# Optimization experiments

Hardware: AMD Instinct MI355X
Metric: run time of the kernel (lower is better)

Reference implementation:

```python
import jax, jax.numpy as jnp
import numpy as np

ITERATIONS = 3


def squash(s):
    # Faithful to the torch code: norm is taken over axis 2 (the labels axis
    # for s_j of shape (B, 1, L, O)), exactly as torch's squash(dim=2) does.
    mag_sq = jnp.sum(s * s, axis=2, keepdims=True)
    mag = jnp.sqrt(mag_sq)
    return mag_sq / (1.0 + mag_sq) * (s / mag)


def setup_inputs() -> dict:
    key = jax.random.key(0)
    kx, kw = jax.random.split(key)
    B, N, P, L, O = 256, 8, 1152, 10, 16
    x = jax.random.normal(kx, (B, N, P), dtype=jnp.float32)
    # nn.Parameter(torch.randn(1, P, L, O, N))
    W = jax.random.normal(kw, (1, P, L, O, N), dtype=jnp.float32)
    return {"x": x, "W": W}


def reference(x, W):
    # x: (B, N, P), W: (1, P, L, O, N)
    _, P, L, O, N = W.shape
    u = jnp.transpose(x, (0, 2, 1))  # (B, P, N)
    # u_hat[b,p,l,o] = sum_n W[0,p,l,o,n] * u[b,p,n]
    u_hat = jnp.einsum('plon,bpn->bplo', W[0], u)  # (B, P, L, O)

    b_ij = jnp.zeros((1, P, L, 1), dtype=u_hat.dtype)
    v_j = None
    for _ in range(ITERATIONS):
        # softmax over a size-1 trailing axis -> all ones (faithful to source)
        c_ij = jax.nn.softmax(b_ij, axis=-1)           # (1, P, L, 1)
        s_j = jnp.sum(c_ij * u_hat, axis=1, keepdims=True)  # (B, 1, L, O)
        v_j = squash(s_j)                               # (B, 1, L, O)
        # agreement: <u_hat, v_j> over output dim, then mean over batch
        agree = jnp.einsum('bplo,blo->bpl', u_hat, v_j[:, 0])  # (B, P, L)
        b_ij = b_ij + jnp.mean(agree, axis=0)[None, :, :, None]
    return jnp.squeeze(v_j)  # (B, L, O)
```

## Files before the change

### kernel.cpp

```cpp
#include <hip/hip_runtime.h>
#include <hip/hip_bf16.h>
#include <math.h>

#define B_TOT 256
#define P_P   1152
#define J_J   160
#define K_K   9216
#define L_L   10

#define SG 18
#define JG 5

typedef __attribute__((ext_vector_type(8))) short short8;
typedef __attribute__((ext_vector_type(4))) float f32x4;

__device__ __forceinline__ short f2bf(float f) {
    __hip_bfloat16 h = __float2bfloat16(f);
    return __builtin_bit_cast(short, h);
}

__global__ __launch_bounds__(256, 4) void gemm_direct(const float* __restrict__ x,
                                                      const float* __restrict__ W,
                                                      float* __restrict__ part) {
    const int bt = blockIdx.x;
    const int sg = blockIdx.y;
    const int jg = blockIdx.z;
    const int tid  = threadIdx.x;
    const int w    = tid >> 6;
    const int lane = tid & 63;
    const int b0 = bt * 32;
    const int p0 = sg * 64;
    const int j0 = jg * 32;

    __shared__ __align__(16) short As[32][520];
    float (*redux)[64][17] = (float (*)[64][17])(&As[0][0]);

    #pragma unroll
    for (int i = 0; i < 8; ++i) {
        const int bb = w * 8 + i;
        const float* xr = x + (size_t)(b0 + bb) * K_K + p0 + lane;
        short8 sh;
        #pragma unroll
        for (int n = 0; n < 8; ++n)
            sh[n] = f2bf(xr[(size_t)n * P_P]);
        *reinterpret_cast<short8*>(&As[bb][lane * 8]) = sh;
    }
    __syncthreads();

    const int m  = lane & 15;
    const int kq = lane >> 4;

    f32x4 acc00 = {0.f,0.f,0.f,0.f}, acc01 = {0.f,0.f,0.f,0.f};
    f32x4 acc10 = {0.f,0.f,0.f,0.f}, acc11 = {0.f,0.f,0.f,0.f};

    const float* wbase = W + (size_t)(p0 + w * 16 + kq) * 1280 + (size_t)(j0 + m) * 8;

    #pragma unroll
    for (int ks = 0; ks < 4; ++ks) {
        const short8 af0 =
            *reinterpret_cast<const short8*>(&As[m][w * 128 + ks * 32 + kq * 8]);
        const short8 af1 =
            *reinterpret_cast<const short8*>(&As[m + 16][w * 128 + ks * 32 + kq * 8]);
        const float* wp = wbase + (size_t)ks * 4 * 1280;
        const f32x4 a0 = *reinterpret_cast<const f32x4*>(wp);
        const f32x4 a1 = *reinterpret_cast<const f32x4*>(wp + 4);
        const f32x4 c0 = *reinterpret_cast<const f32x4*>(wp + 128);
        const f32x4 c1 = *reinterpret_cast<const f32x4*>(wp + 132);
        short8 bf0, bf1;
        #pragma unroll
        for (int e = 0; e < 4; ++e) {
            bf0[e]     = f2bf(a0[e]);
            bf0[e + 4] = f2bf(a1[e]);
            bf1[e]     = f2bf(c0[e]);
            bf1[e + 4] = f2bf(c1[e]);
        }
        acc00 = __builtin_amdgcn_mfma_f32_16x16x32_bf16(af0, bf0, acc00, 0, 0, 0);
        acc01 = __builtin_amdgcn_mfma_f32_16x16x32_bf16(af0, bf1, acc01, 0, 0, 0);
        acc10 = __builtin_amdgcn_mfma_f32_16x16x32_bf16(af1, bf0, acc10, 0, 0, 0);
        acc11 = __builtin_amdgcn_mfma_f32_16x16x32_bf16(af1, bf1, acc11, 0, 0, 0);
    }

    __syncthreads();

    #pragma unroll
    for (int r = 0; r < 4; ++r) {
        redux[w][lane][r]      = acc00[r];
        redux[w][lane][r + 4]  = acc01[r];
        redux[w][lane][r + 8]  = acc10[r];
        redux[w][lane][r + 12] = acc11[r];
    }
    __syncthreads();

    {
        const int bl = tid >> 3;
        const int q  = tid & 7;
        const int ji = q >> 2;
        const int mq = q & 3;
        const int bi  = bl >> 4;
        const int kqd = (bl >> 2) & 3;
        const int r   = bl & 3;
        const int c   = bi * 8 + ji * 4 + r;
        f32x4 v;
        #pragma unroll
        for (int u = 0; u < 4; ++u) {
            const int ln = kqd * 16 + mq * 4 + u;
            v[u] = redux[0][ln][c] + redux[1][ln][c]
                 + redux[2][ln][c] + redux[3][ln][c];
        }
        *reinterpret_cast<f32x4*>(
            &part[((size_t)(b0 + bl) * SG + sg) * J_J + j0 + q * 4]) = v;
    }
}

__global__ __launch_bounds__(128) void reduce_squash(const float* __restrict__ part,
                                                     float* __restrict__ out) {
    const int b   = blockIdx.x;
    const int tid = threadIdx.x;
    __shared__ f32x4 psum[3][40];
    __shared__ float sld[J_J];
    __shared__ float scl[16];

    const f32x4* p4 = reinterpret_cast<const f32x4*>(part + (size_t)b * SG * J_J);
    const int jq  = tid % 40;
    const int sgt = tid / 40;
    if (sgt < 3) {
        f32x4 s = {0.f, 0.f, 0.f, 0.f};
        #pragma unroll
        for (int si = 0; si < 6; ++si)
            s += p4[(sgt * 6 + si) * 40 + jq];
        psum[sgt][jq] = s;
    }
    __syncthreads();
    if (tid < 40) {
        const f32x4 t = psum[0][tid] + psum[1][tid] + psum[2][tid];
        *reinterpret_cast<f32x4*>(&sld[tid * 4]) = t;
    }
    __syncthreads();
    if (tid < 16) {
        float ms = 0.f;
        #pragma unroll
        for (int l = 0; l < L_L; ++l) {
            const float v = sld[l * 16 + tid];
            ms = fmaf(v, v, ms);
        }
        scl[tid] = sqrtf(ms) / (1.0f + ms);
    }
    __syncthreads();
    out[(size_t)b * J_J + tid] = sld[tid] * scl[tid & 15];
    if (tid < 32) {
        const int j = 128 + tid;
        out[(size_t)b * J_J + j] = sld[j] * scl[j & 15];
    }
}

extern "C" void kernel_launch(void* const* d_in, const int* in_sizes, int n_in,
                              void* d_out, int out_size, void* d_ws, size_t ws_size,
                              hipStream_t stream) {
    const float* x = (const float*)d_in[0];
    const float* W = (const float*)d_in[1];
    float* out = (float*)d_out;

    float* part = (float*)d_ws;

    dim3 gg(B_TOT / 32, SG, JG);
    gemm_direct<<<gg, 256, 0, stream>>>(x, W, part);

    reduce_squash<<<B_TOT, 128, 0, stream>>>(part, out);
}
```

Before: 17.72 us.

## Fuse reduce-squash into GEMM kernel via last-block flag synchronization

Removes the second kernel launch. Each GEMM block now publishes its partial sums with atomic stores, then sets per-8-batch group flags in the workspace. Any block that sees all 90 flags of a group set reduces that group's partials over the spatial groups, applies the squash scaling and writes the output, then clears the flags. This saves the launch and the inter-kernel gap, at the cost of extra flag traffic. It relies on relaxed atomics plus an acquire load, and the clearing approach could race, so more than one block might finish the same group.

```diff
diff --git a/kernel.cpp b/kernel.cpp
--- a/kernel.cpp
+++ b/kernel.cpp
@@ -10,6 +10,7 @@
 
 #define SG 18
 #define JG 5
+#define MAGIC 0x5EEDF00Du
 
 typedef __attribute__((ext_vector_type(8))) short short8;
 typedef __attribute__((ext_vector_type(4))) float f32x4;
@@ -19,9 +20,11 @@
     return __builtin_bit_cast(short, h);
 }
 
-__global__ __launch_bounds__(256, 4) void gemm_direct(const float* __restrict__ x,
-                                                      const float* __restrict__ W,
-                                                      float* __restrict__ part) {
+__global__ __launch_bounds__(256, 4) void gemm_fused(const float* __restrict__ x,
+                                                     const float* __restrict__ W,
+                                                     float* __restrict__ part,
+                                                     unsigned* __restrict__ flags,
+                                                     float* __restrict__ out) {
     const int bt = blockIdx.x;
     const int sg = blockIdx.y;
     const int jg = blockIdx.z;
@@ -34,6 +37,7 @@
 
     __shared__ __align__(16) short As[32][520];
     float (*redux)[64][17] = (float (*)[64][17])(&As[0][0]);
+    __shared__ int nall[4];
 
     #pragma unroll
     for (int i = 0; i < 8; ++i) {
@@ -100,56 +104,87 @@
         const int kqd = (bl >> 2) & 3;
         const int r   = bl & 3;
         const int c   = bi * 8 + ji * 4 + r;
-        f32x4 v;
+        float* dst = &part[((size_t)(b0 + bl) * SG + sg) * J_J + j0 + q * 4];
         #pragma unroll
         for (int u = 0; u < 4; ++u) {
             const int ln = kqd * 16 + mq * 4 + u;
-            v[u] = redux[0][ln][c] + redux[1][ln][c]
-                 + redux[2][ln][c] + redux[3][ln][c];
-        }
-        *reinterpret_cast<f32x4*>(
-            &part[((size_t)(b0 + bl) * SG + sg) * J_J + j0 + q * 4]) = v;
-    }
-}
-
-__global__ __launch_bounds__(128) void reduce_squash(const float* __restrict__ part,
-                                                     float* __restrict__ out) {
-    const int b   = blockIdx.x;
-    const int tid = threadIdx.x;
-    __shared__ f32x4 psum[3][40];
-    __shared__ float sld[J_J];
-    __shared__ float scl[16];
-
-    const f32x4* p4 = reinterpret_cast<const f32x4*>(part + (size_t)b * SG * J_J);
-    const int jq  = tid % 40;
-    const int sgt = tid / 40;
-    if (sgt < 3) {
-        f32x4 s = {0.f, 0.f, 0.f, 0.f};
-        #pragma unroll
-        for (int si = 0; si < 6; ++si)
-            s += p4[(sgt * 6 + si) * 40 + jq];
-        psum[sgt][jq] = s;
-    }
-    __syncthreads();
-    if (tid < 40) {
-        const f32x4 t = psum[0][tid] + psum[1][tid] + psum[2][tid];
-        *reinterpret_cast<f32x4*>(&sld[tid * 4]) = t;
-    }
-    __syncthreads();
-    if (tid < 16) {
-        float ms = 0.f;
-        #pragma unroll
-        for (int l = 0; l < L_L; ++l) {
-            const float v = sld[l * 16 + tid];
-            ms = fmaf(v, v, ms);
-        }
-        scl[tid] = sqrtf(ms) / (1.0f + ms);
-    }
-    __syncthreads();
-    out[(size_t)b * J_J + tid] = sld[tid] * scl[tid & 15];
-    if (tid < 32) {
-        const int j = 128 + tid;
-        out[(size_t)b * J_J + j] = sld[j] * scl[j & 15];
+            const float s = redux[0][ln][c] + redux[1][ln][c]
+                          + redux[2][ln][c] + redux[3][ln][c];
+            __hip_atomic_store(dst + u, s, __ATOMIC_RELAXED,
+                               __HIP_MEMORY_SCOPE_AGENT);
+        }
+    }
+    asm volatile("s_waitcnt vmcnt(0)" ::: "memory");
+    __syncthreads();
+
+    if (tid < 4)
+        (void)__hip_atomic_exchange(&flags[(bt * 4 + tid) * 90 + sg * 5 + jg],
+                                    MAGIC, __ATOMIC_RELAXED,
+                                    __HIP_MEMORY_SCOPE_AGENT);
+    asm volatile("s_waitcnt vmcnt(0)" ::: "memory");
+    __syncthreads();
+
+    if (tid < 4) nall[tid] = 0;
+    __syncthreads();
+    #pragma unroll
+    for (int gi = 0; gi < 4; ++gi) {
+        if (tid < 90) {
+            const unsigned v = __hip_atomic_load(
+                &flags[(bt * 4 + gi) * 90 + tid], __ATOMIC_RELAXED,
+                __HIP_MEMORY_SCOPE_AGENT);
+            if (v != MAGIC) nall[gi] = 1;
+        }
+    }
+    __syncthreads();
+    if (nall[0] & nall[1] & nall[2] & nall[3]) return;
+
+    if (tid == 0)
+        (void)__hip_atomic_load(&flags[bt * 4 * 90], __ATOMIC_ACQUIRE,
+                                __HIP_MEMORY_SCOPE_AGENT);
+    __syncthreads();
+
+    float (*sld)[J_J] = (float (*)[J_J])(&As[0][0]);
+    float* scl = (float*)(&As[0][0]) + 8 * J_J;
+    const f32x4* part4 = reinterpret_cast<const f32x4*>(part);
+    f32x4* out4 = reinterpret_cast<f32x4*>(out);
+
+    for (int gi = 0; gi < 4; ++gi) {
+        if (nall[gi]) continue;
+        const int gb = b0 + gi * 8;
+        __syncthreads();
+        for (int u = tid; u < 320; u += 256) {
+            const int bb = u / 40, quad = u - (u / 40) * 40;
+            f32x4 s = {0.f, 0.f, 0.f, 0.f};
+            #pragma unroll
+            for (int si = 0; si < SG; ++si)
+                s += part4[((size_t)(gb + bb) * SG + si) * 40 + quad];
+            *reinterpret_cast<f32x4*>(&sld[bb][quad * 4]) = s;
+        }
+        __syncthreads();
+        if (tid < 128) {
+            const int bb = tid >> 4, o = tid & 15;
+            float ms = 0.f;
+            #pragma unroll
+            for (int l = 0; l < L_L; ++l) {
+                const float v = sld[bb][l * 16 + o];
+                ms = fmaf(v, v, ms);
+            }
+            scl[tid] = sqrtf(ms) / (1.0f + ms);
+        }
+        __syncthreads();
+        for (int u = tid; u < 320; u += 256) {
+            const int bb = u / 40, quad = u - (u / 40) * 40;
+            const f32x4 s = *reinterpret_cast<const f32x4*>(&sld[bb][quad * 4]);
+            f32x4 r;
+            #pragma unroll
+            for (int e = 0; e < 4; ++e)
+                r[e] = s[e] * scl[bb * 16 + ((quad * 4 + e) & 15)];
+            out4[(size_t)(gb + bb) * 40 + quad] = r;
+        }
+        __syncthreads();
+        if (tid < 90)
+            __hip_atomic_store(&flags[(bt * 4 + gi) * 90 + tid], 0u,
+                               __ATOMIC_RELAXED, __HIP_MEMORY_SCOPE_AGENT);
     }
 }
 
@@ -160,10 +195,9 @@
     const float* W = (const float*)d_in[1];
     float* out = (float*)d_out;
 
-    float* part = (float*)d_ws;
+    float*    part  = (float*)d_ws;
+    unsigned* flags = (unsigned*)(part + (size_t)B_TOT * SG * J_J);
 
     dim3 gg(B_TOT / 32, SG, JG);
-    gemm_direct<<<gg, 256, 0, stream>>>(x, W, part);
-
-    reduce_squash<<<B_TOT, 128, 0, stream>>>(part, out);
+    gemm_fused<<<gg, 256, 0, stream>>>(x, W, part, flags, out);
 }
```

Result: slower. 37.42 us (+111.2%).
